# Performance work log

Hardware: AMD Instinct MI355X
Metric: run time of the kernel (lower is better)

The kernel has to match this reference:

```python
import jax, jax.numpy as jnp
import numpy as np

N, SD, VD, ED, E, NG, NA, NB = 512, 256, 128, 128, 262144, 16, 16, 5


def _lin_init(key, fan_in, fan_out):
    # torch.nn.Linear default: U(-1/sqrt(fan_in), 1/sqrt(fan_in)); stored as (in, out)
    lim = 1.0 / np.sqrt(fan_in)
    return jax.random.uniform(key, (fan_in, fan_out), jnp.float32, -lim, lim)


def setup_inputs() -> dict:
    key = jax.random.key(0)
    ks = jax.random.split(key, 20)
    s = jax.random.normal(ks[0], (N, SD), jnp.float32)
    v = jax.random.normal(ks[1], (N, 3, VD), jnp.float32)
    p = jax.random.normal(ks[2], (N, 3), jnp.float32)
    e = jax.random.normal(ks[3], (E, ED), jnp.float32)
    batch = jnp.sort(jax.random.randint(ks[4], (N,), 0, NG))
    edge_index_global = jax.random.randint(ks[5], (2, E), 0, N)
    W_sm = _lin_init(ks[6], SD, SD); b_sm = jnp.zeros((SD,), jnp.float32)
    W_bm = _lin_init(ks[7], ED, SD); b_bm = jnp.zeros((SD,), jnp.float32)
    W_b0 = _lin_init(ks[8], SD + 1, SD); b_b0 = jnp.zeros((SD,), jnp.float32)
    W_b1 = _lin_init(ks[9], SD, NB); b_b1 = jnp.zeros((NB,), jnp.float32)
    W_c = _lin_init(ks[10], VD, 1)  # no bias
    W_a = _lin_init(ks[11], SD, NA); b_a = jnp.zeros((NA,), jnp.float32)
    return {"s": s, "v": v, "p": p, "e": e, "batch": batch,
            "edge_index_global": edge_index_global,
            "W_sm": W_sm, "b_sm": b_sm, "W_bm": W_bm, "b_bm": b_bm,
            "W_b0": W_b0, "b_b0": b_b0, "W_b1": W_b1, "b_b1": b_b1,
            "W_c": W_c, "W_a": W_a, "b_a": b_a}


def reference(s, v, p, e, batch, edge_index_global,
              W_sm, b_sm, W_bm, b_bm, W_b0, b_b0, W_b1, b_b1, W_c, W_a, b_a):
    # shared_mapping: Linear + SiLU
    s = jax.nn.silu(s @ W_sm + b_sm)                      # [N, SD]
    coords_pred = (v @ W_c)[..., 0]                       # [N, 3]
    atoms_pred = s @ W_a + b_a                            # [N, NA]
    j, i = edge_index_global[0], edge_index_global[1]
    n = s.shape[0]
    # coords_param == 'data': coords = p + pred, then per-graph mean centering
    coords_pred = p + coords_pred
    seg_sum = jax.ops.segment_sum(coords_pred, batch, num_segments=NG)
    counts = jax.ops.segment_sum(jnp.ones((n, 1), coords_pred.dtype), batch, num_segments=NG)
    mean = seg_sum / jnp.maximum(counts, 1.0)
    coords_pred = coords_pred - mean[batch]
    # squared pairwise distance per edge
    d = jnp.sum((coords_pred[i] - coords_pred[j]) ** 2, axis=-1, keepdims=True)  # [E, 1]
    # sparse -> dense -> sparse symmetrization of edge features (as in the source)
    e_dense = jnp.zeros((n, n, e.shape[-1]), e.dtype).at[j, i].set(e)
    e_dense = 0.5 * (e_dense + jnp.transpose(e_dense, (1, 0, 2)))
    e_sym = e_dense[j, i]                                 # [E, ED]
    f = s[i] + s[j] + (e_sym @ W_bm + b_bm)               # [E, SD]
    edge = jnp.concatenate([f, d], axis=-1)               # [E, SD+1]
    bonds_pred = jax.nn.silu(edge @ W_b0 + b_b0) @ W_b1 + b_b1  # [E, NB]
    return coords_pred, atoms_pred, bonds_pred
```

## Files before the change

### kernel.cpp

```cpp
#include <hip/hip_runtime.h>
#include <math.h>

#define N_NODES 512
#define SD_ 256
#define VD_ 128
#define ED_ 128
#define NE_ 262144
#define NG_ 16
#define NA_ 16
#define NB_ 5
#define MAXP 131328

typedef __attribute__((ext_vector_type(8))) short bf16x8;
typedef __attribute__((ext_vector_type(4))) float f32x4;

__device__ __forceinline__ float silu_f(float x) { return x / (1.0f + expf(-x)); }
__device__ __forceinline__ float silu_fast(float x) {
    return x * __builtin_amdgcn_rcpf(1.0f + __builtin_amdgcn_exp2f(x * -1.44269504f));
}
__device__ __forceinline__ unsigned short f2bf(float x) {
    unsigned int u = __float_as_uint(x);
    return (unsigned short)((u + 0x7fffu + ((u >> 16) & 1u)) >> 16);
}
__device__ __forceinline__ float bf2f(unsigned short h) {
    return __uint_as_float(((unsigned int)h) << 16);
}
__device__ __forceinline__ unsigned int cvt_pk_bf16(float lo, float hi) {
    unsigned int r;
    asm("v_cvt_pk_bf16_f32 %0, %1, %2" : "=v"(r) : "v"(lo), "v"(hi));
    return r;
}

__device__ __forceinline__ void pack_one(
    const float* __restrict__ W, unsigned short* __restrict__ out, int nkb, int idx)
{
    int l = idx & 63;
    int kb = (idx >> 6) % nkb;
    int mtg = idx / (64 * nkb);
    int m = mtg * 16 + (l & 15);
    int k0 = kb * 32 + (l >> 4) * 8;
    bf16x8 pack;
    #pragma unroll
    for (int i = 0; i < 8; ++i) pack[i] = (short)f2bf(W[(size_t)(k0 + i) * SD_ + m]);
    *(bf16x8*)(out + (size_t)idx * 8) = pack;
}

__global__ __launch_bounds__(256) void prep_a(
    const int* __restrict__ ei, int* __restrict__ emap,
    const float* __restrict__ W_bm, const float* __restrict__ W_b0,
    unsigned short* __restrict__ WfA_bm, unsigned short* __restrict__ WfA_b0,
    const float* __restrict__ s, const float* __restrict__ v, const float* __restrict__ p,
    const float* __restrict__ W_sm, const float* __restrict__ b_sm,
    const float* __restrict__ W_a, const float* __restrict__ b_a,
    const float* __restrict__ W_c,
    unsigned short* __restrict__ s2b, float* __restrict__ cpred, float* __restrict__ atoms_out,
    int* __restrict__ counter, float* __restrict__ zrow)
{
    __shared__ float srow[8][SD_];
    __shared__ float s2row[8][SD_];
    const int bid = blockIdx.x;
    const int tid = threadIdx.x;

    if (bid < 1024) {
        int k = bid * 256 + tid;
        int j = ei[k], i = ei[NE_ + k];
        atomicMax(&emap[j * N_NODES + i], k);
        return;
    }
    if (bid < 1072) {
        int idx = (bid - 1024) * 256 + tid;
        if (idx < 4096)  pack_one(W_bm, WfA_bm, 4, idx);
        else             pack_one(W_b0, WfA_b0, 8, idx - 4096);
        return;
    }
    if (bid < 1136) {
        const int n0 = (bid - 1072) * 8;
        #pragma unroll
        for (int n = 0; n < 8; ++n) srow[n][tid] = s[(size_t)(n0 + n) * SD_ + tid];
        __syncthreads();
        float acc[8];
        {
            float bb = b_sm[tid];
            #pragma unroll
            for (int n = 0; n < 8; ++n) acc[n] = bb;
        }
        #pragma unroll 4
        for (int c = 0; c < SD_; ++c) {
            float wv = W_sm[(size_t)c * SD_ + tid];
            #pragma unroll
            for (int n = 0; n < 8; ++n) acc[n] = fmaf(srow[n][c], wv, acc[n]);
        }
        #pragma unroll
        for (int n = 0; n < 8; ++n) {
            float sv = silu_f(acc[n]);
            s2b[(size_t)(n0 + n) * SD_ + tid] = f2bf(sv);
            s2row[n][tid] = sv;
        }
        __syncthreads();
        if (tid < 128) {
            int n = tid >> 4, a = tid & 15;
            float x = b_a[a];
            #pragma unroll 8
            for (int c = 0; c < SD_; ++c) x = fmaf(s2row[n][c], W_a[(size_t)c * NA_ + a], x);
            atoms_out[(size_t)(n0 + n) * NA_ + a] = x;
        }
        return;
    }
    if (tid == 0) counter[0] = 0;
    if (tid < ED_) zrow[tid] = 0.0f;
    for (int o = tid; o < N_NODES * 3; o += 256) {
        float x = p[o];
        const float* vr = v + (size_t)o * VD_;
        #pragma unroll 8
        for (int c = 0; c < VD_; ++c) x = fmaf(vr[c], W_c[c], x);
        cpred[o] = x;
    }
}

__global__ __launch_bounds__(512) void prep_b(
    const float* __restrict__ cpred, const int* __restrict__ batch,
    float* __restrict__ coords_ws, float* __restrict__ coords_out,
    const int* __restrict__ emap, int* __restrict__ counter,
    int* __restrict__ pairslot, int4* __restrict__ worklist)
{
    __shared__ float cl[N_NODES * 3];
    __shared__ int   bl[N_NODES];
    __shared__ float meanv[NG_ * 3];
    const int tid = threadIdx.x;

    if (blockIdx.x == 0) {
        bl[tid] = batch[tid];
        #pragma unroll
        for (int dd = 0; dd < 3; ++dd) cl[tid * 3 + dd] = cpred[tid * 3 + dd];
        __syncthreads();
        if (tid < NG_ * 3) {
            int g = tid / 3, dd = tid % 3;
            float sum = 0.f; int cnt = 0;
            for (int n = 0; n < N_NODES; ++n) {
                if (bl[n] == g) { sum += cl[n * 3 + dd]; cnt++; }
            }
            meanv[tid] = sum / (float)(cnt > 0 ? cnt : 1);
        }
        __syncthreads();
        int g = bl[tid];
        #pragma unroll
        for (int dd = 0; dd < 3; ++dd) {
            float val = cl[tid * 3 + dd] - meanv[g * 3 + dd];
            coords_ws[tid * 3 + dd]  = val;
            coords_out[tid * 3 + dd] = val;
        }
        return;
    }
    int idx = (blockIdx.x - 1) * 512 + tid;
    int a = idx >> 9, b = idx & (N_NODES - 1);
    bool lower = (a <= b);
    int k1 = -1, k2 = -1;
    if (lower) {
        k1 = emap[(a << 9) | b];
        k2 = emap[(b << 9) | a];
    }
    bool qual = lower && (k1 >= 0 || k2 >= 0);
    unsigned long long mask = __ballot(qual);
    if (mask == 0ull) return;
    int lane = tid & 63;
    int leader = __ffsll((unsigned long long)mask) - 1;
    int base = 0;
    if (lane == leader) base = atomicAdd(counter, __popcll(mask));
    base = __shfl(base, leader);
    if (qual) {
        int slot = base + __popcll(mask & ((1ull << lane) - 1ull));
        pairslot[(a << 9) | b] = slot;
        pairslot[(b << 9) | a] = slot;
        worklist[slot] = make_int4(a, b, k1, k2);
    }
}

__global__ __launch_bounds__(256) void bonds_scatter(
    const int* __restrict__ ei, const int* __restrict__ pairslot,
    const float* __restrict__ repval, float* __restrict__ bonds_out)
{
    int k = blockIdx.x * 256 + threadIdx.x;
    int j = ei[k], i = ei[NE_ + k];
    int slot = pairslot[(j << 9) | i];
    const float* rp = repval + (size_t)slot * NB_;
    #pragma unroll
    for (int b = 0; b < NB_; ++b)
        bonds_out[(size_t)k * NB_ + b] = rp[b];
}

__global__ __launch_bounds__(512) void edge_mfma(
    const float* __restrict__ e, const int4* __restrict__ worklist,
    const int* __restrict__ counter, const float* __restrict__ coords,
    const float* __restrict__ zrow, const unsigned short* __restrict__ s2b,
    const unsigned short* __restrict__ WfA_bm, const unsigned short* __restrict__ WfA_b0,
    const float* __restrict__ W_b1,
    const float* __restrict__ b_bm, const float* __restrict__ W_b0_last,
    const float* __restrict__ b_b0, const float* __restrict__ b_b1,
    float* __restrict__ repval)
{
    const int blk = blockIdx.x;
    const int cnt = counter[0];
    if (blk * 64 >= cnt) return;

    __shared__ __align__(16) char smem0[64 * 128 * 2];
    __shared__ __align__(16) unsigned short fd_lds[64 * 256];
    __shared__ unsigned short wb1t[NB_ * 256];
    __shared__ float dw[64];
    __shared__ int li_s[64], lj_s[64];

    unsigned short* esym_lds   = (unsigned short*)smem0;
    float*          bonds_part = (float*)smem0;

    const int tid = threadIdx.x;
    const int l   = tid & 63;
    const int w   = tid >> 6;
    const int eLo = l & 15;
    const int hi  = l >> 4;

    bf16x8 a1pf[4][2];
    #pragma unroll
    for (int kb = 0; kb < 4; ++kb)
        #pragma unroll
        for (int mt = 0; mt < 2; ++mt)
            a1pf[kb][mt] = *(const bf16x8*)(WfA_bm + ((size_t)(((w * 2 + mt) * 4 + kb) * 64 + l) * 8));

    if (tid < 256) {
        const int eL = l;
        const int q  = w;
        int widx = min(blk * 64 + eL, cnt - 1);
        int4 wk = worklist[widx];
        const float* r1 = (wk.z >= 0) ? (e + (size_t)wk.z * ED_) : zrow;
        const float* r2 = (wk.w >= 0) ? (e + (size_t)wk.w * ED_) : zrow;
        const float4* p1 = (const float4*)(r1 + q * 32);
        const float4* p2 = (const float4*)(r2 + q * 32);
        float4 va[8], vb[8];
        #pragma unroll
        for (int t = 0; t < 8; ++t) va[t] = p1[t];
        #pragma unroll
        for (int t = 0; t < 8; ++t) vb[t] = p2[t];
        #pragma unroll
        for (int t = 0; t < 8; ++t) {
            va[t].x += vb[t].x; va[t].y += vb[t].y;
            va[t].z += vb[t].z; va[t].w += vb[t].w;
        }
        int ntB = eL >> 4, eLoB = eL & 15;
        #pragma unroll
        for (int h2 = 0; h2 < 4; ++h2) {
            float4 x0 = va[h2 * 2], x1 = va[h2 * 2 + 1];
            uint4 c;
            c.x = cvt_pk_bf16(0.5f * x0.x, 0.5f * x0.y);
            c.y = cvt_pk_bf16(0.5f * x0.z, 0.5f * x0.w);
            c.z = cvt_pk_bf16(0.5f * x1.x, 0.5f * x1.y);
            c.w = cvt_pk_bf16(0.5f * x1.z, 0.5f * x1.w);
            int chunk = (ntB * 4 + q) * 64 + h2 * 16 + eLoB;
            *(uint4*)(&esym_lds[chunk * 8]) = c;
        }
    } else {
        int t = tid - 256;
        #pragma unroll
        for (int b = 0; b < NB_; ++b)
            wb1t[b * 256 + t] = f2bf(W_b1[(size_t)t * NB_ + b]);
        if (t < 64) {
            int widx = min(blk * 64 + t, cnt - 1);
            int4 wk = worklist[widx];
            li_s[t] = wk.x; lj_s[t] = wk.y;
            float dx = coords[wk.x * 3 + 0] - coords[wk.y * 3 + 0];
            float dy = coords[wk.x * 3 + 1] - coords[wk.y * 3 + 1];
            float dz = coords[wk.x * 3 + 2] - coords[wk.y * 3 + 2];
            dw[t] = dx * dx + dy * dy + dz * dz;
        }
    }

    __syncthreads();

    f32x4 acc[2][4];
    #pragma unroll
    for (int mt = 0; mt < 2; ++mt)
        #pragma unroll
        for (int nt = 0; nt < 4; ++nt) acc[mt][nt] = (f32x4){0.f, 0.f, 0.f, 0.f};

    #pragma unroll
    for (int kb = 0; kb < 4; ++kb) {
        bf16x8 bfg[4];
        #pragma unroll
        for (int nt = 0; nt < 4; ++nt)
            bfg[nt] = *(const bf16x8*)(&esym_lds[(size_t)((nt * 4 + kb) * 64 + l) * 8]);
        __builtin_amdgcn_s_setprio(1);
        #pragma unroll
        for (int mt = 0; mt < 2; ++mt)
            #pragma unroll
            for (int nt = 0; nt < 4; ++nt)
                acc[mt][nt] = __builtin_amdgcn_mfma_f32_16x16x32_bf16(a1pf[kb][mt], bfg[nt], acc[mt][nt], 0, 0, 0);
        __builtin_amdgcn_s_setprio(0);
    }

    bf16x8 a2pf[3][2];
    #pragma unroll
    for (int kb = 0; kb < 3; ++kb)
        #pragma unroll
        for (int mt = 0; mt < 2; ++mt)
            a2pf[kb][mt] = *(const bf16x8*)(WfA_b0 + ((size_t)(((w * 2 + mt) * 8 + kb) * 64 + l) * 8));

    #pragma unroll
    for (int mt = 0; mt < 2; ++mt) {
        int m0 = w * 32 + mt * 16 + hi * 4;
        float4 bb = *(const float4*)(b_bm + m0);
        #pragma unroll
        for (int nt = 0; nt < 4; ++nt) {
            int edge = nt * 16 + eLo;
            int ni = li_s[edge], nj = lj_s[edge];
            ushort4 si = *(const ushort4*)(s2b + (size_t)ni * SD_ + m0);
            ushort4 sj = *(const ushort4*)(s2b + (size_t)nj * SD_ + m0);
            f32x4 r = acc[mt][nt];
            float f0 = r[0] + bf2f(si.x) + bf2f(sj.x) + bb.x;
            float f1 = r[1] + bf2f(si.y) + bf2f(sj.y) + bb.y;
            float f2 = r[2] + bf2f(si.z) + bf2f(sj.z) + bb.z;
            float f3 = r[3] + bf2f(si.w) + bf2f(sj.w) + bb.w;
            uint2 pk;
            pk.x = cvt_pk_bf16(f0, f1);
            pk.y = cvt_pk_bf16(f2, f3);
            int c16 = m0 >> 3;
            int byteo = (edge << 9) + ((c16 ^ (edge & 7)) << 4) + ((m0 & 7) << 1);
            *(uint2*)((char*)fd_lds + byteo) = pk;
        }
    }
    __syncthreads();

    #pragma unroll
    for (int mt = 0; mt < 2; ++mt) {
        int m0 = w * 32 + mt * 16 + hi * 4;
        float4 b0 = *(const float4*)(b_b0 + m0);
        float4 w2 = *(const float4*)(W_b0_last + m0);
        #pragma unroll
        for (int nt = 0; nt < 4; ++nt) {
            float dd = dw[nt * 16 + eLo];
            acc[mt][nt] = (f32x4){fmaf(dd, w2.x, b0.x), fmaf(dd, w2.y, b0.y),
                                  fmaf(dd, w2.z, b0.z), fmaf(dd, w2.w, b0.w)};
        }
    }
    #pragma unroll
    for (int kb = 0; kb < 8; ++kb) {
        bf16x8 af[2], bfg[4];
        #pragma unroll
        for (int mt = 0; mt < 2; ++mt)
            af[mt] = (kb < 3) ? a2pf[kb][mt]
                   : *(const bf16x8*)(WfA_b0 + ((size_t)(((w * 2 + mt) * 8 + kb) * 64 + l) * 8));
        #pragma unroll
        for (int nt = 0; nt < 4; ++nt) {
            int edge = nt * 16 + eLo;
            int c16 = (kb << 2) + hi;
            int byteo = (edge << 9) + ((c16 ^ (edge & 7)) << 4);
            bfg[nt] = *(const bf16x8*)((const char*)fd_lds + byteo);
        }
        __builtin_amdgcn_s_setprio(1);
        #pragma unroll
        for (int mt = 0; mt < 2; ++mt)
            #pragma unroll
            for (int nt = 0; nt < 4; ++nt)
                acc[mt][nt] = __builtin_amdgcn_mfma_f32_16x16x32_bf16(af[mt], bfg[nt], acc[mt][nt], 0, 0, 0);
        __builtin_amdgcn_s_setprio(0);
    }

    float pb[4][NB_];
    #pragma unroll
    for (int nt = 0; nt < 4; ++nt)
        #pragma unroll
        for (int b = 0; b < NB_; ++b) pb[nt][b] = 0.f;
    #pragma unroll
    for (int mt = 0; mt < 2; ++mt) {
        int m0 = w * 32 + mt * 16 + hi * 4;
        ushort4 wv[NB_];
        #pragma unroll
        for (int b = 0; b < NB_; ++b)
            wv[b] = *(const ushort4*)(wb1t + b * 256 + m0);
        #pragma unroll
        for (int nt = 0; nt < 4; ++nt) {
            f32x4 r = acc[mt][nt];
            float h0 = silu_fast(r[0]);
            float h1 = silu_fast(r[1]);
            float h2 = silu_fast(r[2]);
            float h3 = silu_fast(r[3]);
            #pragma unroll
            for (int b = 0; b < NB_; ++b) {
                float t = fmaf(h0, bf2f(wv[b].x), fmaf(h1, bf2f(wv[b].y),
                          fmaf(h2, bf2f(wv[b].z), h3 * bf2f(wv[b].w))));
                pb[nt][b] += t;
            }
        }
    }
    #pragma unroll
    for (int off = 16; off <= 32; off <<= 1)
        #pragma unroll
        for (int nt = 0; nt < 4; ++nt)
            #pragma unroll
            for (int b = 0; b < NB_; ++b)
                pb[nt][b] += __shfl_xor(pb[nt][b], off);

    __syncthreads();
    if (hi == 0) {
        #pragma unroll
        for (int nt = 0; nt < 4; ++nt)
            #pragma unroll
            for (int b = 0; b < NB_; ++b)
                bonds_part[(size_t)(w * 64 + nt * 16 + eLo) * NB_ + b] = pb[nt][b];
    }
    __syncthreads();

    for (int idx = tid; idx < 64 * NB_; idx += 512) {
        int edge = idx / NB_, b = idx % NB_;
        float s8 = 0.f;
        #pragma unroll
        for (int pp = 0; pp < 8; ++pp)
            s8 += bonds_part[(size_t)(pp * 64 + edge) * NB_ + b];
        repval[(size_t)(blk * 64 + edge) * NB_ + b] = s8 + b_b1[b];
    }
}

extern "C" void kernel_launch(void* const* d_in, const int* in_sizes, int n_in,
                              void* d_out, int out_size, void* d_ws, size_t ws_size,
                              hipStream_t stream)
{
    const float* s    = (const float*)d_in[0];
    const float* v    = (const float*)d_in[1];
    const float* p    = (const float*)d_in[2];
    const float* e    = (const float*)d_in[3];
    const int*   batch= (const int*)d_in[4];
    const int*   ei   = (const int*)d_in[5];
    const float* W_sm = (const float*)d_in[6];
    const float* b_sm = (const float*)d_in[7];
    const float* W_bm = (const float*)d_in[8];
    const float* b_bm = (const float*)d_in[9];
    const float* W_b0 = (const float*)d_in[10];
    const float* b_b0 = (const float*)d_in[11];
    const float* W_b1 = (const float*)d_in[12];
    const float* b_b1 = (const float*)d_in[13];
    const float* W_c  = (const float*)d_in[14];
    const float* W_a  = (const float*)d_in[15];
    const float* b_a  = (const float*)d_in[16];

    float* out = (float*)d_out;
    float* coords_out = out;
    float* atoms_out  = out + 1536;
    float* bonds_out  = out + 1536 + 8192;

    char* ws = (char*)d_ws;
    int*            emap    = (int*)ws;
    unsigned short* s2b     = (unsigned short*)(ws + 0x100000);
    unsigned short* WfA_bm  = (unsigned short*)(ws + 0x140000);
    unsigned short* WfA_b0  = (unsigned short*)(ws + 0x150000);
    float*          cpred   = (float*)(ws + 0x170000);
    float*          coords  = (float*)(ws + 0x172000);
    int*            counter = (int*)(ws + 0x175000);
    float*          zrow    = (float*)(ws + 0x175100);
    int*            pairslot= (int*)(ws + 0x180000);
    int4*           worklist= (int4*)(ws + 0x280000);
    float*          repval  = (float*)(ws + 0x4B0000);

    prep_a<<<1137, 256, 0, stream>>>(ei, emap, W_bm, W_b0, WfA_bm, WfA_b0,
                                     s, v, p, W_sm, b_sm, W_a, b_a, W_c,
                                     s2b, cpred, atoms_out, counter, zrow);
    prep_b<<<513, 512, 0, stream>>>(cpred, batch, coords, coords_out,
                                    emap, counter, pairslot, worklist);

    edge_mfma<<<(MAXP + 63) / 64, 512, 0, stream>>>(e, worklist, counter, coords, zrow, s2b,
                                                    WfA_bm, WfA_b0, W_b1,
                                                    b_bm, W_b0 + 256 * SD_, b_b0, b_b1,
                                                    repval);
    bonds_scatter<<<NE_ / 256, 256, 0, stream>>>(ei, pairslot, repval, bonds_out);
}
```

Measured before the change: 142.8 us.

## Fold W_bm into W_b0 and precompute per-node S2W to drop second GEMM

Algebraically merges the two chained linear layers: the edge-feature projection W_bm is premultiplied into W_b0 (WfF), and the node term s@W_b0 is precomputed per node (S2W) along with a combined bias, so the per-edge kernel runs only one K=128 MFMA GEMM instead of K=128 plus K=256. Squared distances move to a separate small kernel. This removes the intermediate bf16 activation staging and the larger second GEMM per edge. In exchange it adds prep work (a 256x256x128 weight fusion and a 512x256x256 node GEMM in scalar FMA) and an extra kernel launch, and changes rounding because the fused weights are quantized to bf16.

```diff
diff --git a/kernel.cpp b/kernel.cpp
--- a/kernel.cpp
+++ b/kernel.cpp
@@ -31,30 +31,17 @@
     return r;
 }
 
-__device__ __forceinline__ void pack_one(
-    const float* __restrict__ W, unsigned short* __restrict__ out, int nkb, int idx)
-{
-    int l = idx & 63;
-    int kb = (idx >> 6) % nkb;
-    int mtg = idx / (64 * nkb);
-    int m = mtg * 16 + (l & 15);
-    int k0 = kb * 32 + (l >> 4) * 8;
-    bf16x8 pack;
-    #pragma unroll
-    for (int i = 0; i < 8; ++i) pack[i] = (short)f2bf(W[(size_t)(k0 + i) * SD_ + m]);
-    *(bf16x8*)(out + (size_t)idx * 8) = pack;
-}
-
 __global__ __launch_bounds__(256) void prep_a(
     const int* __restrict__ ei, int* __restrict__ emap,
     const float* __restrict__ W_bm, const float* __restrict__ W_b0,
-    unsigned short* __restrict__ WfA_bm, unsigned short* __restrict__ WfA_b0,
+    unsigned short* __restrict__ WfF,
     const float* __restrict__ s, const float* __restrict__ v, const float* __restrict__ p,
     const float* __restrict__ W_sm, const float* __restrict__ b_sm,
     const float* __restrict__ W_a, const float* __restrict__ b_a,
     const float* __restrict__ W_c,
-    unsigned short* __restrict__ s2b, float* __restrict__ cpred, float* __restrict__ atoms_out,
-    int* __restrict__ counter, float* __restrict__ zrow)
+    const float* __restrict__ b_bm, const float* __restrict__ b_b0,
+    float* __restrict__ s2f, float* __restrict__ cpred, float* __restrict__ atoms_out,
+    int* __restrict__ counter, float* __restrict__ zrow, float* __restrict__ bias2)
 {
     __shared__ float srow[8][SD_];
     __shared__ float s2row[8][SD_];
@@ -67,14 +54,30 @@
         atomicMax(&emap[j * N_NODES + i], k);
         return;
     }
-    if (bid < 1072) {
-        int idx = (bid - 1024) * 256 + tid;
-        if (idx < 4096)  pack_one(W_bm, WfA_bm, 4, idx);
-        else             pack_one(W_b0, WfA_b0, 8, idx - 4096);
+    if (bid < 1040) {
+        int mtg = bid - 1024;
+        int kb = tid >> 6;
+        int l  = tid & 63;
+        int m  = mtg * 16 + (l & 15);
+        int k0 = kb * 32 + (l >> 4) * 8;
+        float a8[8];
+        #pragma unroll
+        for (int i = 0; i < 8; ++i) a8[i] = 0.f;
+        for (int c = 0; c < SD_; ++c) {
+            float wb0 = W_b0[(size_t)c * SD_ + m];
+            #pragma unroll
+            for (int i = 0; i < 8; ++i)
+                a8[i] = fmaf(W_bm[(size_t)(k0 + i) * SD_ + c], wb0, a8[i]);
+        }
+        bf16x8 pack;
+        #pragma unroll
+        for (int i = 0; i < 8; ++i) pack[i] = (short)f2bf(a8[i]);
+        int idx = (mtg * 4 + kb) * 64 + l;
+        *(bf16x8*)(WfF + (size_t)idx * 8) = pack;
         return;
     }
-    if (bid < 1136) {
-        const int n0 = (bid - 1072) * 8;
+    if (bid < 1104) {
+        const int n0 = (bid - 1040) * 8;
         #pragma unroll
         for (int n = 0; n < 8; ++n) srow[n][tid] = s[(size_t)(n0 + n) * SD_ + tid];
         __syncthreads();
@@ -93,7 +96,7 @@
         #pragma unroll
         for (int n = 0; n < 8; ++n) {
             float sv = silu_f(acc[n]);
-            s2b[(size_t)(n0 + n) * SD_ + tid] = f2bf(sv);
+            s2f[(size_t)(n0 + n) * SD_ + tid] = sv;
             s2row[n][tid] = sv;
         }
         __syncthreads();
@@ -106,14 +109,23 @@
         }
         return;
     }
-    if (tid == 0) counter[0] = 0;
-    if (tid < ED_) zrow[tid] = 0.0f;
-    for (int o = tid; o < N_NODES * 3; o += 256) {
-        float x = p[o];
-        const float* vr = v + (size_t)o * VD_;
-        #pragma unroll 8
-        for (int c = 0; c < VD_; ++c) x = fmaf(vr[c], W_c[c], x);
-        cpred[o] = x;
+    if (bid == 1104) {
+        if (tid == 0) counter[0] = 0;
+        if (tid < ED_) zrow[tid] = 0.0f;
+        for (int o = tid; o < N_NODES * 3; o += 256) {
+            float x = p[o];
+            const float* vr = v + (size_t)o * VD_;
+            #pragma unroll 8
+            for (int c = 0; c < VD_; ++c) x = fmaf(vr[c], W_c[c], x);
+            cpred[o] = x;
+        }
+        return;
+    }
+    {
+        float acc = b_b0[tid];
+        for (int c = 0; c < SD_; ++c)
+            acc = fmaf(b_bm[c], W_b0[(size_t)c * SD_ + tid], acc);
+        bias2[tid] = acc;
     }
 }
 
@@ -121,14 +133,17 @@
     const float* __restrict__ cpred, const int* __restrict__ batch,
     float* __restrict__ coords_ws, float* __restrict__ coords_out,
     const int* __restrict__ emap, int* __restrict__ counter,
-    int* __restrict__ pairslot, int4* __restrict__ worklist)
+    int* __restrict__ pairslot, int4* __restrict__ worklist,
+    const float* __restrict__ s2f, const float* __restrict__ W_b0,
+    float* __restrict__ S2W)
 {
     __shared__ float cl[N_NODES * 3];
     __shared__ int   bl[N_NODES];
     __shared__ float meanv[NG_ * 3];
     const int tid = threadIdx.x;
-
-    if (blockIdx.x == 0) {
+    const int bid = blockIdx.x;
+
+    if (bid == 0) {
         bl[tid] = batch[tid];
         #pragma unroll
         for (int dd = 0; dd < 3; ++dd) cl[tid * 3 + dd] = cpred[tid * 3 + dd];
@@ -151,27 +166,45 @@
         }
         return;
     }
-    int idx = (blockIdx.x - 1) * 512 + tid;
-    int a = idx >> 9, b = idx & (N_NODES - 1);
-    bool lower = (a <= b);
-    int k1 = -1, k2 = -1;
-    if (lower) {
-        k1 = emap[(a << 9) | b];
-        k2 = emap[(b << 9) | a];
-    }
-    bool qual = lower && (k1 >= 0 || k2 >= 0);
-    unsigned long long mask = __ballot(qual);
-    if (mask == 0ull) return;
-    int lane = tid & 63;
-    int leader = __ffsll((unsigned long long)mask) - 1;
-    int base = 0;
-    if (lane == leader) base = atomicAdd(counter, __popcll(mask));
-    base = __shfl(base, leader);
-    if (qual) {
-        int slot = base + __popcll(mask & ((1ull << lane) - 1ull));
-        pairslot[(a << 9) | b] = slot;
-        pairslot[(b << 9) | a] = slot;
-        worklist[slot] = make_int4(a, b, k1, k2);
+    if (bid <= 512) {
+        int idx = (bid - 1) * 512 + tid;
+        int a = idx >> 9, b = idx & (N_NODES - 1);
+        bool lower = (a <= b);
+        int k1 = -1, k2 = -1;
+        if (lower) {
+            k1 = emap[(a << 9) | b];
+            k2 = emap[(b << 9) | a];
+        }
+        bool qual = lower && (k1 >= 0 || k2 >= 0);
+        unsigned long long mask = __ballot(qual);
+        if (mask == 0ull) return;
+        int lane = tid & 63;
+        int leader = __ffsll((unsigned long long)mask) - 1;
+        int base = 0;
+        if (lane == leader) base = atomicAdd(counter, __popcll(mask));
+        base = __shfl(base, leader);
+        if (qual) {
+            int slot = base + __popcll(mask & ((1ull << lane) - 1ull));
+            pairslot[(a << 9) | b] = slot;
+            pairslot[(b << 9) | a] = slot;
+            worklist[slot] = make_int4(a, b, k1, k2);
+        }
+        return;
+    }
+    {
+        __shared__ float srows[2][SD_];
+        int n0 = (bid - 513) * 2;
+        if (tid < 512) {
+            int n = tid >> 8, c = tid & 255;
+            srows[n][c] = s2f[(size_t)(n0 + n) * SD_ + c];
+        }
+        __syncthreads();
+        int n = tid >> 8, m = tid & 255;
+        float acc = 0.f;
+        #pragma unroll 8
+        for (int c = 0; c < SD_; ++c)
+            acc = fmaf(srows[n][c], W_b0[(size_t)c * SD_ + m], acc);
+        S2W[(size_t)(n0 + n) * SD_ + m] = acc;
     }
 }
 
@@ -190,26 +223,22 @@
 
 __global__ __launch_bounds__(512) void edge_mfma(
     const float* __restrict__ e, const int4* __restrict__ worklist,
-    const int* __restrict__ counter, const float* __restrict__ coords,
-    const float* __restrict__ zrow, const unsigned short* __restrict__ s2b,
-    const unsigned short* __restrict__ WfA_bm, const unsigned short* __restrict__ WfA_b0,
-    const float* __restrict__ W_b1,
-    const float* __restrict__ b_bm, const float* __restrict__ W_b0_last,
-    const float* __restrict__ b_b0, const float* __restrict__ b_b1,
+    const int* __restrict__ counter, const float* __restrict__ zrow,
+    const unsigned short* __restrict__ WfF, const float* __restrict__ S2W,
+    const float* __restrict__ bias2,
+    const float* __restrict__ W_b1, const float* __restrict__ W_b0_last,
+    const float* __restrict__ b_b1,
     float* __restrict__ repval)
 {
     const int blk = blockIdx.x;
     const int cnt = counter[0];
     if (blk * 64 >= cnt) return;
 
-    __shared__ __align__(16) char smem0[64 * 128 * 2];
-    __shared__ __align__(16) unsigned short fd_lds[64 * 256];
+    __shared__ __align__(16) unsigned short esym_lds[64 * 128];
     __shared__ unsigned short wb1t[NB_ * 256];
+    __shared__ float bonds_part[8 * 64 * NB_];
     __shared__ float dw[64];
     __shared__ int li_s[64], lj_s[64];
-
-    unsigned short* esym_lds   = (unsigned short*)smem0;
-    float*          bonds_part = (float*)smem0;
 
     const int tid = threadIdx.x;
     const int l   = tid & 63;
@@ -222,7 +251,7 @@
     for (int kb = 0; kb < 4; ++kb)
         #pragma unroll
         for (int mt = 0; mt < 2; ++mt)
-            a1pf[kb][mt] = *(const bf16x8*)(WfA_bm + ((size_t)(((w * 2 + mt) * 4 + kb) * 64 + l) * 8));
+            a1pf[kb][mt] = *(const bf16x8*)(WfF + ((size_t)(((w * 2 + mt) * 4 + kb) * 64 + l) * 8));
 
     if (tid < 256) {
         const int eL = l;
@@ -231,29 +260,33 @@
         int4 wk = worklist[widx];
         const float* r1 = (wk.z >= 0) ? (e + (size_t)wk.z * ED_) : zrow;
         const float* r2 = (wk.w >= 0) ? (e + (size_t)wk.w * ED_) : zrow;
-        const float4* p1 = (const float4*)(r1 + q * 32);
-        const float4* p2 = (const float4*)(r2 + q * 32);
-        float4 va[8], vb[8];
-        #pragma unroll
-        for (int t = 0; t < 8; ++t) va[t] = p1[t];
-        #pragma unroll
-        for (int t = 0; t < 8; ++t) vb[t] = p2[t];
-        #pragma unroll
-        for (int t = 0; t < 8; ++t) {
-            va[t].x += vb[t].x; va[t].y += vb[t].y;
-            va[t].z += vb[t].z; va[t].w += vb[t].w;
-        }
         int ntB = eL >> 4, eLoB = eL & 15;
         #pragma unroll
-        for (int h2 = 0; h2 < 4; ++h2) {
-            float4 x0 = va[h2 * 2], x1 = va[h2 * 2 + 1];
-            uint4 c;
-            c.x = cvt_pk_bf16(0.5f * x0.x, 0.5f * x0.y);
-            c.y = cvt_pk_bf16(0.5f * x0.z, 0.5f * x0.w);
-            c.z = cvt_pk_bf16(0.5f * x1.x, 0.5f * x1.y);
-            c.w = cvt_pk_bf16(0.5f * x1.z, 0.5f * x1.w);
-            int chunk = (ntB * 4 + q) * 64 + h2 * 16 + eLoB;
-            *(uint4*)(&esym_lds[chunk * 8]) = c;
+        for (int half = 0; half < 2; ++half) {
+            const float4* p1 = (const float4*)(r1 + q * 32 + half * 16);
+            const float4* p2 = (const float4*)(r2 + q * 32 + half * 16);
+            float4 va[4], vb[4];
+            #pragma unroll
+            for (int t = 0; t < 4; ++t) va[t] = p1[t];
+            #pragma unroll
+            for (int t = 0; t < 4; ++t) vb[t] = p2[t];
+            #pragma unroll
+            for (int t = 0; t < 4; ++t) {
+                va[t].x += vb[t].x; va[t].y += vb[t].y;
+                va[t].z += vb[t].z; va[t].w += vb[t].w;
+            }
+            #pragma unroll
+            for (int t = 0; t < 2; ++t) {
+                float4 x0 = va[t * 2], x1 = va[t * 2 + 1];
+                uint4 c;
+                c.x = cvt_pk_bf16(0.5f * x0.x, 0.5f * x0.y);
+                c.y = cvt_pk_bf16(0.5f * x0.z, 0.5f * x0.w);
+                c.z = cvt_pk_bf16(0.5f * x1.x, 0.5f * x1.y);
+                c.w = cvt_pk_bf16(0.5f * x1.z, 0.5f * x1.w);
+                int h2 = half * 2 + t;
+                int chunk = (ntB * 4 + q) * 64 + h2 * 16 + eLoB;
+                *(uint4*)(&esym_lds[chunk * 8]) = c;
+            }
         }
     } else {
         int t = tid - 256;
@@ -264,10 +297,12 @@
             int widx = min(blk * 64 + t, cnt - 1);
             int4 wk = worklist[widx];
             li_s[t] = wk.x; lj_s[t] = wk.y;
-            float dx = coords[wk.x * 3 + 0] - coords[wk.y * 3 + 0];
-            float dy = coords[wk.x * 3 + 1] - coords[wk.y * 3 + 1];
-            float dz = coords[wk.x * 3 + 2] - coords[wk.y * 3 + 2];
-            dw[t] = dx * dx + dy * dy + dz * dz;
+        }
+        if (t >= 64 && t < 128) {
+            int t2 = t - 64;
+            int widx = min(blk * 64 + t2, cnt - 1);
+            int4 wk = worklist[widx];
+            li_s[t2] = wk.x; lj_s[t2] = wk.y;
         }
     }
 
@@ -275,9 +310,23 @@
 
     f32x4 acc[2][4];
     #pragma unroll
-    for (int mt = 0; mt < 2; ++mt)
-        #pragma unroll
-        for (int nt = 0; nt < 4; ++nt) acc[mt][nt] = (f32x4){0.f, 0.f, 0.f, 0.f};
+    for (int mt = 0; mt < 2; ++mt) {
+        int m0 = w * 32 + mt * 16 + hi * 4;
+        float4 bz = *(const float4*)(bias2 + m0);
+        float4 w2 = *(const float4*)(W_b0_last + m0);
+        #pragma unroll
+        for (int nt = 0; nt < 4; ++nt) {
+            int pair = nt * 16 + eLo;
+            int na = li_s[pair], nb2 = lj_s[pair];
+            float4 sa  = *(const float4*)(S2W + (size_t)na  * SD_ + m0);
+            float4 sb4 = *(const float4*)(S2W + (size_t)nb2 * SD_ + m0);
+            float dd = dw[pair];
+            acc[mt][nt] = (f32x4){fmaf(dd, w2.x, bz.x) + sa.x + sb4.x,
+                                  fmaf(dd, w2.y, bz.y) + sa.y + sb4.y,
+                                  fmaf(dd, w2.z, bz.z) + sa.z + sb4.z,
+                                  fmaf(dd, w2.w, bz.w) + sa.w + sb4.w};
+        }
+    }
 
     #pragma unroll
     for (int kb = 0; kb < 4; ++kb) {
@@ -291,73 +340,6 @@
             #pragma unroll
             for (int nt = 0; nt < 4; ++nt)
                 acc[mt][nt] = __builtin_amdgcn_mfma_f32_16x16x32_bf16(a1pf[kb][mt], bfg[nt], acc[mt][nt], 0, 0, 0);
-        __builtin_amdgcn_s_setprio(0);
-    }
-
-    bf16x8 a2pf[3][2];
-    #pragma unroll
-    for (int kb = 0; kb < 3; ++kb)
-        #pragma unroll
-        for (int mt = 0; mt < 2; ++mt)
-            a2pf[kb][mt] = *(const bf16x8*)(WfA_b0 + ((size_t)(((w * 2 + mt) * 8 + kb) * 64 + l) * 8));
-
-    #pragma unroll
-    for (int mt = 0; mt < 2; ++mt) {
-        int m0 = w * 32 + mt * 16 + hi * 4;
-        float4 bb = *(const float4*)(b_bm + m0);
-        #pragma unroll
-        for (int nt = 0; nt < 4; ++nt) {
-            int edge = nt * 16 + eLo;
-            int ni = li_s[edge], nj = lj_s[edge];
-            ushort4 si = *(const ushort4*)(s2b + (size_t)ni * SD_ + m0);
-            ushort4 sj = *(const ushort4*)(s2b + (size_t)nj * SD_ + m0);
-            f32x4 r = acc[mt][nt];
-            float f0 = r[0] + bf2f(si.x) + bf2f(sj.x) + bb.x;
-            float f1 = r[1] + bf2f(si.y) + bf2f(sj.y) + bb.y;
-            float f2 = r[2] + bf2f(si.z) + bf2f(sj.z) + bb.z;
-            float f3 = r[3] + bf2f(si.w) + bf2f(sj.w) + bb.w;
-            uint2 pk;
-            pk.x = cvt_pk_bf16(f0, f1);
-            pk.y = cvt_pk_bf16(f2, f3);
-            int c16 = m0 >> 3;
-            int byteo = (edge << 9) + ((c16 ^ (edge & 7)) << 4) + ((m0 & 7) << 1);
-            *(uint2*)((char*)fd_lds + byteo) = pk;
-        }
-    }
-    __syncthreads();
-
-    #pragma unroll
-    for (int mt = 0; mt < 2; ++mt) {
-        int m0 = w * 32 + mt * 16 + hi * 4;
-        float4 b0 = *(const float4*)(b_b0 + m0);
-        float4 w2 = *(const float4*)(W_b0_last + m0);
-        #pragma unroll
-        for (int nt = 0; nt < 4; ++nt) {
-            float dd = dw[nt * 16 + eLo];
-            acc[mt][nt] = (f32x4){fmaf(dd, w2.x, b0.x), fmaf(dd, w2.y, b0.y),
-                                  fmaf(dd, w2.z, b0.z), fmaf(dd, w2.w, b0.w)};
-        }
-    }
-    #pragma unroll
-    for (int kb = 0; kb < 8; ++kb) {
-        bf16x8 af[2], bfg[4];
-        #pragma unroll
-        for (int mt = 0; mt < 2; ++mt)
-            af[mt] = (kb < 3) ? a2pf[kb][mt]
-                   : *(const bf16x8*)(WfA_b0 + ((size_t)(((w * 2 + mt) * 8 + kb) * 64 + l) * 8));
-        #pragma unroll
-        for (int nt = 0; nt < 4; ++nt) {
-            int edge = nt * 16 + eLo;
-            int c16 = (kb << 2) + hi;
-            int byteo = (edge << 9) + ((c16 ^ (edge & 7)) << 4);
-            bfg[nt] = *(const bf16x8*)((const char*)fd_lds + byteo);
-        }
-        __builtin_amdgcn_s_setprio(1);
-        #pragma unroll
-        for (int mt = 0; mt < 2; ++mt)
-            #pragma unroll
-            for (int nt = 0; nt < 4; ++nt)
-                acc[mt][nt] = __builtin_amdgcn_mfma_f32_16x16x32_bf16(af[mt], bfg[nt], acc[mt][nt], 0, 0, 0);
         __builtin_amdgcn_s_setprio(0);
     }
 
@@ -395,8 +377,190 @@
             #pragma unroll
             for (int b = 0; b < NB_; ++b)
                 pb[nt][b] += __shfl_xor(pb[nt][b], off);
-
+    if (hi == 0) {
+        #pragma unroll
+        for (int nt = 0; nt < 4; ++nt)
+            #pragma unroll
+            for (int b = 0; b < NB_; ++b)
+                bonds_part[(size_t)(w * 64 + nt * 16 + eLo) * NB_ + b] = pb[nt][b];
+    }
     __syncthreads();
+
+    for (int idx = tid; idx < 64 * NB_; idx += 512) {
+        int edge = idx / NB_, b = idx % NB_;
+        float s8 = 0.f;
+        #pragma unroll
+        for (int pp = 0; pp < 8; ++pp)
+            s8 += bonds_part[(size_t)(pp * 64 + edge) * NB_ + b];
+        repval[(size_t)(blk * 64 + edge) * NB_ + b] = s8 + b_b1[b];
+    }
+}
+
+__global__ __launch_bounds__(256) void pair_dsq(
+    const int4* __restrict__ worklist, const int* __restrict__ counter,
+    const float* __restrict__ coords, float* __restrict__ dsq)
+{
+    int idx = blockIdx.x * 256 + threadIdx.x;
+    int cnt = counter[0];
+    if (idx >= cnt) return;
+    int4 wk = worklist[idx];
+    float dx = coords[wk.x * 3 + 0] - coords[wk.y * 3 + 0];
+    float dy = coords[wk.x * 3 + 1] - coords[wk.y * 3 + 1];
+    float dz = coords[wk.x * 3 + 2] - coords[wk.y * 3 + 2];
+    dsq[idx] = dx * dx + dy * dy + dz * dz;
+}
+
+__global__ __launch_bounds__(512) void edge_mfma2(
+    const float* __restrict__ e, const int4* __restrict__ worklist,
+    const int* __restrict__ counter, const float* __restrict__ zrow,
+    const unsigned short* __restrict__ WfF, const float* __restrict__ S2W,
+    const float* __restrict__ bias2, const float* __restrict__ dsq,
+    const float* __restrict__ W_b1, const float* __restrict__ W_b0_last,
+    const float* __restrict__ b_b1,
+    float* __restrict__ repval)
+{
+    const int blk = blockIdx.x;
+    const int cnt = counter[0];
+    if (blk * 64 >= cnt) return;
+
+    __shared__ __align__(16) unsigned short esym_lds[64 * 128];
+    __shared__ unsigned short wb1t[NB_ * 256];
+    __shared__ float bonds_part[8 * 64 * NB_];
+    __shared__ float dw[64];
+    __shared__ int li_s[64], lj_s[64];
+
+    const int tid = threadIdx.x;
+    const int l   = tid & 63;
+    const int w   = tid >> 6;
+    const int eLo = l & 15;
+    const int hi  = l >> 4;
+
+    bf16x8 a1pf[4][2];
+    #pragma unroll
+    for (int kb = 0; kb < 4; ++kb)
+        #pragma unroll
+        for (int mt = 0; mt < 2; ++mt)
+            a1pf[kb][mt] = *(const bf16x8*)(WfF + ((size_t)(((w * 2 + mt) * 4 + kb) * 64 + l) * 8));
+
+    if (tid < 256) {
+        const int eL = l;
+        const int q  = w;
+        int widx = min(blk * 64 + eL, cnt - 1);
+        int4 wk = worklist[widx];
+        const float* r1 = (wk.z >= 0) ? (e + (size_t)wk.z * ED_) : zrow;
+        const float* r2 = (wk.w >= 0) ? (e + (size_t)wk.w * ED_) : zrow;
+        int ntB = eL >> 4, eLoB = eL & 15;
+        #pragma unroll
+        for (int half = 0; half < 2; ++half) {
+            const float4* p1 = (const float4*)(r1 + q * 32 + half * 16);
+            const float4* p2 = (const float4*)(r2 + q * 32 + half * 16);
+            float4 va[4], vb[4];
+            #pragma unroll
+            for (int t = 0; t < 4; ++t) va[t] = p1[t];
+            #pragma unroll
+            for (int t = 0; t < 4; ++t) vb[t] = p2[t];
+            #pragma unroll
+            for (int t = 0; t < 4; ++t) {
+                va[t].x += vb[t].x; va[t].y += vb[t].y;
+                va[t].z += vb[t].z; va[t].w += vb[t].w;
+            }
+            #pragma unroll
+            for (int t = 0; t < 2; ++t) {
+                float4 x0 = va[t * 2], x1 = va[t * 2 + 1];
+                uint4 c;
+                c.x = cvt_pk_bf16(0.5f * x0.x, 0.5f * x0.y);
+                c.y = cvt_pk_bf16(0.5f * x0.z, 0.5f * x0.w);
+                c.z = cvt_pk_bf16(0.5f * x1.x, 0.5f * x1.y);
+                c.w = cvt_pk_bf16(0.5f * x1.z, 0.5f * x1.w);
+                int h2 = half * 2 + t;
+                int chunk = (ntB * 4 + q) * 64 + h2 * 16 + eLoB;
+                *(uint4*)(&esym_lds[chunk * 8]) = c;
+            }
+        }
+    } else {
+        int t = tid - 256;
+        #pragma unroll
+        for (int b = 0; b < NB_; ++b)
+            wb1t[b * 256 + t] = f2bf(W_b1[(size_t)t * NB_ + b]);
+        if (t < 64) {
+            int widx = min(blk * 64 + t, cnt - 1);
+            int4 wk = worklist[widx];
+            li_s[t] = wk.x; lj_s[t] = wk.y;
+            dw[t] = dsq[widx];
+        }
+    }
+
+    __syncthreads();
+
+    f32x4 acc[2][4];
+    #pragma unroll
+    for (int mt = 0; mt < 2; ++mt) {
+        int m0 = w * 32 + mt * 16 + hi * 4;
+        float4 bz = *(const float4*)(bias2 + m0);
+        float4 w2 = *(const float4*)(W_b0_last + m0);
+        #pragma unroll
+        for (int nt = 0; nt < 4; ++nt) {
+            int pair = nt * 16 + eLo;
+            int na = li_s[pair], nb2 = lj_s[pair];
+            float4 sa  = *(const float4*)(S2W + (size_t)na  * SD_ + m0);
+            float4 sb4 = *(const float4*)(S2W + (size_t)nb2 * SD_ + m0);
+            float dd = dw[pair];
+            acc[mt][nt] = (f32x4){fmaf(dd, w2.x, bz.x) + sa.x + sb4.x,
+                                  fmaf(dd, w2.y, bz.y) + sa.y + sb4.y,
+                                  fmaf(dd, w2.z, bz.z) + sa.z + sb4.z,
+                                  fmaf(dd, w2.w, bz.w) + sa.w + sb4.w};
+        }
+    }
+
+    #pragma unroll
+    for (int kb = 0; kb < 4; ++kb) {
+        bf16x8 bfg[4];
+        #pragma unroll
+        for (int nt = 0; nt < 4; ++nt)
+            bfg[nt] = *(const bf16x8*)(&esym_lds[(size_t)((nt * 4 + kb) * 64 + l) * 8]);
+        __builtin_amdgcn_s_setprio(1);
+        #pragma unroll
+        for (int mt = 0; mt < 2; ++mt)
+            #pragma unroll
+            for (int nt = 0; nt < 4; ++nt)
+                acc[mt][nt] = __builtin_amdgcn_mfma_f32_16x16x32_bf16(a1pf[kb][mt], bfg[nt], acc[mt][nt], 0, 0, 0);
+        __builtin_amdgcn_s_setprio(0);
+    }
+
+    float pb[4][NB_];
+    #pragma unroll
+    for (int nt = 0; nt < 4; ++nt)
+        #pragma unroll
+        for (int b = 0; b < NB_; ++b) pb[nt][b] = 0.f;
+    #pragma unroll
+    for (int mt = 0; mt < 2; ++mt) {
+        int m0 = w * 32 + mt * 16 + hi * 4;
+        ushort4 wv[NB_];
+        #pragma unroll
+        for (int b = 0; b < NB_; ++b)
+            wv[b] = *(const ushort4*)(wb1t + b * 256 + m0);
+        #pragma unroll
+        for (int nt = 0; nt < 4; ++nt) {
+            f32x4 r = acc[mt][nt];
+            float h0 = silu_fast(r[0]);
+            float h1 = silu_fast(r[1]);
+            float h2 = silu_fast(r[2]);
+            float h3 = silu_fast(r[3]);
+            #pragma unroll
+            for (int b = 0; b < NB_; ++b) {
+                float t = fmaf(h0, bf2f(wv[b].x), fmaf(h1, bf2f(wv[b].y),
+                          fmaf(h2, bf2f(wv[b].z), h3 * bf2f(wv[b].w))));
+                pb[nt][b] += t;
+            }
+        }
+    }
+    #pragma unroll
+    for (int off = 16; off <= 32; off <<= 1)
+        #pragma unroll
+        for (int nt = 0; nt < 4; ++nt)
+            #pragma unroll
+            for (int b = 0; b < NB_; ++b)
+                pb[nt][b] += __shfl_xor(pb[nt][b], off);
     if (hi == 0) {
         #pragma unroll
         for (int nt = 0; nt < 4; ++nt)
@@ -445,26 +609,31 @@
 
     char* ws = (char*)d_ws;
     int*            emap    = (int*)ws;
-    unsigned short* s2b     = (unsigned short*)(ws + 0x100000);
-    unsigned short* WfA_bm  = (unsigned short*)(ws + 0x140000);
-    unsigned short* WfA_b0  = (unsigned short*)(ws + 0x150000);
-    float*          cpred   = (float*)(ws + 0x170000);
-    float*          coords  = (float*)(ws + 0x172000);
-    int*            counter = (int*)(ws + 0x175000);
-    float*          zrow    = (float*)(ws + 0x175100);
-    int*            pairslot= (int*)(ws + 0x180000);
-    int4*           worklist= (int4*)(ws + 0x280000);
-    float*          repval  = (float*)(ws + 0x4B0000);
-
-    prep_a<<<1137, 256, 0, stream>>>(ei, emap, W_bm, W_b0, WfA_bm, WfA_b0,
+    float*          s2f     = (float*)(ws + 0x100000);
+    unsigned short* WfF     = (unsigned short*)(ws + 0x180000);
+    float*          S2W     = (float*)(ws + 0x190000);
+    float*          bias2   = (float*)(ws + 0x210000);
+    float*          cpred   = (float*)(ws + 0x211000);
+    float*          coords  = (float*)(ws + 0x213000);
+    int*            counter = (int*)(ws + 0x215000);
+    float*          zrow    = (float*)(ws + 0x215100);
+    float*          dsq     = (float*)(ws + 0x216000);
+    int*            pairslot= (int*)(ws + 0x2A0000);
+    int4*           worklist= (int4*)(ws + 0x3A0000);
+    float*          repval  = (float*)(ws + 0x5D0000);
+
+    prep_a<<<1106, 256, 0, stream>>>(ei, emap, W_bm, W_b0, WfF,
                                      s, v, p, W_sm, b_sm, W_a, b_a, W_c,
-                                     s2b, cpred, atoms_out, counter, zrow);
-    prep_b<<<513, 512, 0, stream>>>(cpred, batch, coords, coords_out,
-                                    emap, counter, pairslot, worklist);
-
-    edge_mfma<<<(MAXP + 63) / 64, 512, 0, stream>>>(e, worklist, counter, coords, zrow, s2b,
-                                                    WfA_bm, WfA_b0, W_b1,
-                                                    b_bm, W_b0 + 256 * SD_, b_b0, b_b1,
-                                                    repval);
+                                     b_bm, b_b0,
+                                     s2f, cpred, atoms_out, counter, zrow, bias2);
+    prep_b<<<769, 512, 0, stream>>>(cpred, batch, coords, coords_out,
+                                    emap, counter, pairslot, worklist,
+                                    s2f, W_b0, S2W);
+    pair_dsq<<<(MAXP + 255) / 256, 256, 0, stream>>>(worklist, counter, coords, dsq);
+
+    edge_mfma2<<<(MAXP + 63) / 64, 512, 0, stream>>>(e, worklist, counter, zrow,
+                                                     WfF, S2W, bias2, dsq,
+                                                     W_b1, W_b0 + 256 * SD_, b_b1,
+                                                     repval);
     bonds_scatter<<<NE_ / 256, 256, 0, stream>>>(ei, pairslot, repval, bonds_out);
 }
```

Result: faster. 132.1 us (-7.5%).
